# Kernel tuning notes

Measured on AMD Instinct MI355X. Metric: run time of the kernel, lower is better.

## Reference

```python
import jax, jax.numpy as jnp
import numpy as np

DIM = 768
HEADS = 12
FF = 3072
EPS = 1e-6


def setup_inputs() -> dict:
    key = jax.random.key(0)
    ks = jax.random.split(key, 12)
    B, S, D, F_ = 64, 197, DIM, FF
    s = 0.02
    inp = {
        "x": jax.random.normal(ks[0], (B, S, D), jnp.float32),
        "Wq": jax.random.normal(ks[1], (D, D), jnp.float32) * s,
        "bq": jnp.zeros((D,), jnp.float32),
        "Wk": jax.random.normal(ks[2], (D, D), jnp.float32) * s,
        "bk": jnp.zeros((D,), jnp.float32),
        "Wv": jax.random.normal(ks[3], (D, D), jnp.float32) * s,
        "bv": jnp.zeros((D,), jnp.float32),
        "Wo": jax.random.normal(ks[4], (D, D), jnp.float32) * s,
        "bo": jnp.zeros((D,), jnp.float32),
        "ln1_w": jnp.ones((D,), jnp.float32),
        "ln1_b": jnp.zeros((D,), jnp.float32),
        "W1": jax.random.normal(ks[5], (D, F_), jnp.float32) * s,
        "b1": jnp.zeros((F_,), jnp.float32),
        "W2": jax.random.normal(ks[6], (F_, D), jnp.float32) * s,
        "b2": jnp.zeros((D,), jnp.float32),
        "ln2_w": jnp.ones((D,), jnp.float32),
        "ln2_b": jnp.zeros((D,), jnp.float32),
        "mask": jnp.ones((B, S), jnp.int32),
    }
    return inp


def _layernorm(x, w, b):
    m = jnp.mean(x, axis=-1, keepdims=True)
    v = jnp.mean(jnp.square(x - m), axis=-1, keepdims=True)  # unbiased=False
    return (x - m) / jnp.sqrt(v + EPS) * w + b


def _block(x, mask_f, Wq, bq, Wk, bk, Wv, bv, Wo, bo, ln1_w, ln1_b, W1, b1, W2, b2, ln2_w, ln2_b):
    B, S, D = x.shape
    H = HEADS
    Dh = D // H
    # --- attention (pre-norm) ---
    h = _layernorm(x, ln1_w, ln1_b)
    q = (h @ Wq + bq).reshape(B, S, H, Dh).transpose(0, 2, 1, 3)
    k = (h @ Wk + bk).reshape(B, S, H, Dh).transpose(0, 2, 1, 3)
    v = (h @ Wv + bv).reshape(B, S, H, Dh).transpose(0, 2, 1, 3)
    scores = jnp.einsum("bhqd,bhkd->bhqk", q, k) / jnp.sqrt(jnp.float32(Dh))
    scores = scores - 10000.0 * (1.0 - mask_f[:, None, None, :])
    probs = jax.nn.softmax(scores, axis=-1)
    attn = jnp.einsum("bhqk,bhkd->bhqd", probs, v).transpose(0, 2, 1, 3).reshape(B, S, D)
    x = x + (attn @ Wo + bo)  # dropout = identity (eval)
    # --- FFN (pre-norm), exact erf GELU (F.gelu default) ---
    h = _layernorm(x, ln2_w, ln2_b)
    h = jax.nn.gelu(h @ W1 + b1, approximate=False)
    x = x + (h @ W2 + b2)
    return x


def reference(x, Wq, bq, Wk, bk, Wv, bv, Wo, bo, ln1_w, ln1_b, W1, b1, W2, b2, ln2_w, ln2_b, mask):
    mask_f = mask.astype(jnp.float32)
    return _block(x, mask_f, Wq, bq, Wk, bk, Wv, bv, Wo, bo, ln1_w, ln1_b, W1, b1, W2, b2, ln2_w, ln2_b)
```

## Files before the change

### kernel.cpp

```cpp
#include <hip/hip_runtime.h>
#include <stdint.h>

#define B_   64
#define S_   197
#define D_   768
#define H_   12
#define F_   3072
#define BS_  (B_ * S_)

typedef __attribute__((ext_vector_type(8))) short short8;
typedef __attribute__((ext_vector_type(4))) float f32x4;

__device__ __forceinline__ float bf2f(unsigned short h) {
    union { unsigned int u; float f; } v; v.u = ((unsigned int)h) << 16; return v.f;
}
__device__ __forceinline__ unsigned short f2bf(float f) {
    union { float f; unsigned int u; } v; v.f = f;
    unsigned int r = v.u + 0x7FFFu + ((v.u >> 16) & 1u);
    return (unsigned short)(r >> 16);
}

__device__ __forceinline__ void g2l16(const void* g, void* l) {
    __builtin_amdgcn_global_load_lds(
        (const __attribute__((address_space(1))) unsigned int*)g,
        (__attribute__((address_space(3))) unsigned int*)l, 16, 0, 0);
}

__global__ __launch_bounds__(256)
void transpose_w(const float* __restrict__ W, unsigned short* __restrict__ Wt, int K, int N) {
    __shared__ float t[32][33];
    int n0 = blockIdx.x * 32, k0 = blockIdx.y * 32;
    int tx = threadIdx.x, ty = threadIdx.y;
#pragma unroll
    for (int i = ty; i < 32; i += 8) t[i][tx] = W[(size_t)(k0 + i) * N + n0 + tx];
    __syncthreads();
#pragma unroll
    for (int i = ty; i < 32; i += 8) Wt[(size_t)(n0 + i) * K + k0 + tx] = f2bf(t[tx][i]);
}

__global__ void biascat_kernel(const float* bq, const float* bk, const float* bv, float* o) {
    int i = blockIdx.x * 256 + threadIdx.x;
    if (i < 2304) o[i] = i < 768 ? bq[i] : (i < 1536 ? bk[i - 768] : bv[i - 1536]);
}

__global__ __launch_bounds__(256)
void ln_kernel(const float* __restrict__ x, const float* __restrict__ w,
               const float* __restrict__ b, unsigned short* __restrict__ out) {
    int row = blockIdx.x; size_t base = (size_t)row * 768;
    int tid = threadIdx.x;
    float v0 = x[base + tid], v1 = x[base + tid + 256], v2 = x[base + tid + 512];
    float s1 = v0 + v1 + v2;
    float s2 = v0 * v0 + v1 * v1 + v2 * v2;
#pragma unroll
    for (int off = 32; off > 0; off >>= 1) { s1 += __shfl_xor(s1, off); s2 += __shfl_xor(s2, off); }
    __shared__ float sa[4], sb[4];
    int w4 = tid >> 6;
    if ((tid & 63) == 0) { sa[w4] = s1; sb[w4] = s2; }
    __syncthreads();
    s1 = sa[0] + sa[1] + sa[2] + sa[3];
    s2 = sb[0] + sb[1] + sb[2] + sb[3];
    float mean = s1 * (1.f / 768.f);
    float var  = s2 * (1.f / 768.f) - mean * mean;
    float rstd = rsqrtf(var + 1e-6f);
    out[base + tid]       = f2bf((v0 - mean) * rstd * w[tid]       + b[tid]);
    out[base + tid + 256] = f2bf((v1 - mean) * rstd * w[tid + 256] + b[tid + 256]);
    out[base + tid + 512] = f2bf((v2 - mean) * rstd * w[tid + 512] + b[tid + 512]);
}

template<int MODE>
__global__ __launch_bounds__(256)
void gemm_bf16(const unsigned short* __restrict__ A, const unsigned short* __restrict__ Bt,
               const float* __restrict__ bias, const float* __restrict__ resid,
               void* __restrict__ out, int M, int N, int K) {
    __shared__ unsigned short As[128 * 32];
    __shared__ unsigned short Bs[128 * 32];
    const int tid = threadIdx.x;
    const int l = tid & 63, w = tid >> 6;
    const int lr = l & 15, lg = l >> 4;
    const int wr = w >> 1, wc = w & 1;
    const int bm0 = blockIdx.y * 128, bn0 = blockIdx.x * 128;

    f32x4 acc[4][4];
#pragma unroll
    for (int i = 0; i < 4; ++i)
#pragma unroll
        for (int j = 0; j < 4; ++j) acc[i][j] = (f32x4){0.f, 0.f, 0.f, 0.f};

    for (int k0 = 0; k0 < K; k0 += 32) {
        __syncthreads();
#pragma unroll
        for (int p = 0; p < 2; ++p) {
            int r0 = p * 64 + w * 16;
            int ra = bm0 + r0 + (l >> 2); ra = ra < M ? ra : M - 1;
            g2l16(A + (size_t)ra * K + k0 + (l & 3) * 8, &As[r0 * 32]);
            int rb = bn0 + r0 + (l >> 2);
            g2l16(Bt + (size_t)rb * K + k0 + (l & 3) * 8, &Bs[r0 * 32]);
        }
        __syncthreads();
        short8 af[4], bfr[4];
#pragma unroll
        for (int i = 0; i < 4; ++i) af[i]  = *(const short8*)&As[(wr * 64 + i * 16 + lr) * 32 + lg * 8];
#pragma unroll
        for (int j = 0; j < 4; ++j) bfr[j] = *(const short8*)&Bs[(wc * 64 + j * 16 + lr) * 32 + lg * 8];
#pragma unroll
        for (int i = 0; i < 4; ++i)
#pragma unroll
            for (int j = 0; j < 4; ++j)
                acc[i][j] = __builtin_amdgcn_mfma_f32_16x16x32_bf16(af[i], bfr[j], acc[i][j], 0, 0, 0);
    }
#pragma unroll
    for (int i = 0; i < 4; ++i)
#pragma unroll
        for (int j = 0; j < 4; ++j)
#pragma unroll
            for (int r = 0; r < 4; ++r) {
                int gm = bm0 + wr * 64 + i * 16 + lg * 4 + r;
                int gn = bn0 + wc * 64 + j * 16 + lr;
                if (gm < M) {
                    float c = acc[i][j][r] + bias[gn];
                    if (MODE == 0) {
                        if (gn < 768) c *= 0.125f;
                        ((unsigned short*)out)[(size_t)gm * N + gn] = f2bf(c);
                    } else if (MODE == 1) {
                        ((float*)out)[(size_t)gm * N + gn] = c + resid[(size_t)gm * N + gn];
                    } else {
                        float g = 0.5f * c * (1.f + erff(c * 0.70710678118f));
                        ((unsigned short*)out)[(size_t)gm * N + gn] = f2bf(g);
                    }
                }
            }
}

__global__ __launch_bounds__(256)
void attn_mfma(const unsigned short* __restrict__ qkv, const int* __restrict__ mask,
               unsigned short* __restrict__ ctx) {
    __shared__ unsigned short Ks[208 * 64];
    __shared__ unsigned short Vt[64 * 256];
    __shared__ unsigned short Psl[4][16 * 40];
    __shared__ float maskadj[224];
    const int bh = blockIdx.x, b = bh / 12, h = bh - b * 12;
    const int tid = threadIdx.x, l = tid & 63, w = tid >> 6;
    const int lr = l & 15, lg = l >> 4;
    const unsigned short* Qg = qkv + (size_t)b * 197 * 2304 + h * 64;
    const unsigned short* Kg = Qg + 768;
    const unsigned short* Vg = Qg + 1536;

    if (tid < 224)
        maskadj[tid] = tid < 197 ? -10000.f * (1.f - (float)mask[b * 197 + tid]) : -1e30f;

    for (int c = w; c < 26; c += 4) {
        int row = c * 8 + (l >> 3);
        int rc = row < 197 ? row : 196;
        int blk = (l & 7) ^ (row & 7);
        g2l16(Kg + (size_t)rc * 2304 + blk * 8, &Ks[c * 8 * 64]);
    }
    {
        int jj = tid >> 3, db = tid & 7;
#pragma unroll
        for (int it = 0; it < 7; ++it) {
            int j = it * 32 + jj;
            short8 v = (short8){0, 0, 0, 0, 0, 0, 0, 0};
            if (j < 197) v = *(const short8*)(Vg + (size_t)j * 2304 + db * 8);
#pragma unroll
            for (int e = 0; e < 8; ++e) {
                int d = db * 8 + e;
                Vt[d * 256 + (((j >> 3) ^ (d & 7)) * 8) + (j & 7)] = (unsigned short)v[e];
            }
        }
    }
    __syncthreads();

    for (int t = w; t < 13; t += 4) {
        const int q0 = t * 16;
        int qr = q0 + lr; qr = qr < 197 ? qr : 196;
        const short8 qf0 = *(const short8*)(Qg + (size_t)qr * 2304 + lg * 8);
        const short8 qf1 = *(const short8*)(Qg + (size_t)qr * 2304 + 32 + lg * 8);

        f32x4 sc[13];
#pragma unroll
        for (int kt = 0; kt < 13; ++kt) {
            const int krow = kt * 16 + lr;
            const short8 kf0 = *(const short8*)&Ks[krow * 64 + ((lg ^ (lr & 7)) * 8)];
            const short8 kf1 = *(const short8*)&Ks[krow * 64 + (((4 + lg) ^ (lr & 7)) * 8)];
            f32x4 a = (f32x4){0.f, 0.f, 0.f, 0.f};
            a = __builtin_amdgcn_mfma_f32_16x16x32_bf16(qf0, kf0, a, 0, 0, 0);
            a = __builtin_amdgcn_mfma_f32_16x16x32_bf16(qf1, kf1, a, 0, 0, 0);
            sc[kt] = a;
        }
        float mx[4] = {-1e30f, -1e30f, -1e30f, -1e30f};
#pragma unroll
        for (int kt = 0; kt < 13; ++kt) {
            float ma = maskadj[kt * 16 + lr];
#pragma unroll
            for (int r = 0; r < 4; ++r) {
                sc[kt][r] += ma;
                mx[r] = fmaxf(mx[r], sc[kt][r]);
            }
        }
#pragma unroll
        for (int r = 0; r < 4; ++r) {
            mx[r] = fmaxf(mx[r], __shfl_xor(mx[r], 1));
            mx[r] = fmaxf(mx[r], __shfl_xor(mx[r], 2));
            mx[r] = fmaxf(mx[r], __shfl_xor(mx[r], 4));
            mx[r] = fmaxf(mx[r], __shfl_xor(mx[r], 8));
        }
        float sm[4] = {0.f, 0.f, 0.f, 0.f};
#pragma unroll
        for (int kt = 0; kt < 13; ++kt)
#pragma unroll
            for (int r = 0; r < 4; ++r) {
                float p = __expf(sc[kt][r] - mx[r]);
                sc[kt][r] = p;
                sm[r] += p;
            }
#pragma unroll
        for (int r = 0; r < 4; ++r) {
            sm[r] += __shfl_xor(sm[r], 1);
            sm[r] += __shfl_xor(sm[r], 2);
            sm[r] += __shfl_xor(sm[r], 4);
            sm[r] += __shfl_xor(sm[r], 8);
            sm[r] = 1.f / sm[r];
        }
        f32x4 ao[4];
#pragma unroll
        for (int dt = 0; dt < 4; ++dt) ao[dt] = (f32x4){0.f, 0.f, 0.f, 0.f};
        unsigned short* Pw = &Psl[w][0];
#pragma unroll
        for (int ks = 0; ks < 7; ++ks) {
#pragma unroll
            for (int tl = 0; tl < 2; ++tl) {
                const int kt = ks * 2 + tl;
#pragma unroll
                for (int r = 0; r < 4; ++r) {
                    unsigned short pv = 0;
                    if (kt < 13) pv = f2bf(sc[kt][r] * sm[r]);
                    Pw[(lg * 4 + r) * 40 + tl * 16 + lr] = pv;
                }
            }
            const short8 pf = *(const short8*)&Pw[lr * 40 + lg * 8];
#pragma unroll
            for (int dt = 0; dt < 4; ++dt) {
                const int drow = dt * 16 + lr;
                const short8 vf = *(const short8*)&Vt[drow * 256 + (((4 * ks + lg) ^ (lr & 7)) * 8)];
                ao[dt] = __builtin_amdgcn_mfma_f32_16x16x32_bf16(vf, pf, ao[dt], 0, 0, 0);
            }
        }
        const int q = q0 + lr;
        if (q < 197) {
            unsigned short* crow = ctx + ((size_t)b * 197 + q) * 768 + h * 64;
#pragma unroll
            for (int dt = 0; dt < 4; ++dt) {
                union { unsigned short u[4]; uint2 v; } pk;
#pragma unroll
                for (int r = 0; r < 4; ++r) pk.u[r] = f2bf(ao[dt][r]);
                *(uint2*)(crow + dt * 16 + lg * 4) = pk.v;
            }
        }
    }
}

extern "C" void kernel_launch(void* const* d_in, const int* in_sizes, int n_in,
                              void* d_out, int out_size, void* d_ws, size_t ws_size,
                              hipStream_t stream) {
    const float* x    = (const float*)d_in[0];
    const float* Wq   = (const float*)d_in[1];
    const float* bq   = (const float*)d_in[2];
    const float* Wk   = (const float*)d_in[3];
    const float* bk   = (const float*)d_in[4];
    const float* Wv   = (const float*)d_in[5];
    const float* bv   = (const float*)d_in[6];
    const float* Wo   = (const float*)d_in[7];
    const float* bo   = (const float*)d_in[8];
    const float* ln1w = (const float*)d_in[9];
    const float* ln1b = (const float*)d_in[10];
    const float* W1   = (const float*)d_in[11];
    const float* b1   = (const float*)d_in[12];
    const float* W2   = (const float*)d_in[13];
    const float* b2   = (const float*)d_in[14];
    const float* ln2w = (const float*)d_in[15];
    const float* ln2b = (const float*)d_in[16];
    const int*   mask = (const int*)d_in[17];

    size_t off = 0;
    auto nxt = [&](size_t bytes) -> void* {
        void* r = (char*)d_ws + off; off += (bytes + 255) & ~(size_t)255; return r;
    };
    unsigned short* hbuf  = (unsigned short*)nxt((size_t)BS_ * 768 * 2);
    unsigned short* qkvg  = (unsigned short*)nxt((size_t)BS_ * 3072 * 2);
    unsigned short* wqkvT = (unsigned short*)nxt((size_t)2304 * 768 * 2);
    unsigned short* woT   = (unsigned short*)nxt((size_t)768 * 768 * 2);
    unsigned short* w1T   = (unsigned short*)nxt((size_t)3072 * 768 * 2);
    unsigned short* w2T   = (unsigned short*)nxt((size_t)768 * 3072 * 2);
    float*          bcat  = (float*)nxt(2304 * 4);
    unsigned short* ctx   = (unsigned short*)nxt((size_t)BS_ * 768 * 2);
    (void)ws_size; (void)in_sizes; (void)n_in; (void)out_size;

    dim3 t32(32, 8, 1);
    transpose_w<<<dim3(24, 24), t32, 0, stream>>>(Wq, wqkvT,                 768, 768);
    transpose_w<<<dim3(24, 24), t32, 0, stream>>>(Wk, wqkvT + 768 * 768,     768, 768);
    transpose_w<<<dim3(24, 24), t32, 0, stream>>>(Wv, wqkvT + 2 * 768 * 768, 768, 768);
    transpose_w<<<dim3(24, 24), t32, 0, stream>>>(Wo, woT,                   768, 768);
    transpose_w<<<dim3(96, 24), t32, 0, stream>>>(W1, w1T,                   768, 3072);
    transpose_w<<<dim3(24, 96), t32, 0, stream>>>(W2, w2T,                   3072, 768);
    biascat_kernel<<<9, 256, 0, stream>>>(bq, bk, bv, bcat);

    ln_kernel<<<BS_, 256, 0, stream>>>(x, ln1w, ln1b, hbuf);
    gemm_bf16<0><<<dim3(18, 99), 256, 0, stream>>>(hbuf, wqkvT, bcat, nullptr, qkvg, BS_, 2304, 768);
    attn_mfma<<<768, 256, 0, stream>>>(qkvg, mask, ctx);
    gemm_bf16<1><<<dim3(6, 99), 256, 0, stream>>>(ctx, woT, bo, x, d_out, BS_, 768, 768);
    ln_kernel<<<BS_, 256, 0, stream>>>((const float*)d_out, ln2w, ln2b, hbuf);
    gemm_bf16<2><<<dim3(24, 99), 256, 0, stream>>>(hbuf, w1T, b1, nullptr, qkvg, BS_, 3072, 768);
    gemm_bf16<1><<<dim3(6, 99), 256, 0, stream>>>(qkvg, w2T, b2, (const float*)d_out, d_out, BS_, 768, 3072);
}
```

Measured before the change: 506.6 us.

## Double-buffer GEMM LDS tiles, swizzle LDS, remap XCDs, fuse weight prep kernels

The GEMM now uses two LDS buffers so the global-to-LDS load of the next K tile can overlap the MFMA work on the current one. It also XOR-swizzles the LDS column blocks to cut bank conflicts and remaps workgroup IDs so neighbouring M tiles land on the same XCD, which should improve L2 reuse of B tiles. Separately, the seven weight-transpose and bias-concat launches are merged into one kernel to reduce launch overhead. The cost is doubled LDS per block, which may lower occupancy, and a single sync per iteration that relies on the async load finishing in order.

```diff
diff --git a/kernel.cpp b/kernel.cpp
--- a/kernel.cpp
+++ b/kernel.cpp
@@ -27,20 +27,38 @@
 }
 
 __global__ __launch_bounds__(256)
-void transpose_w(const float* __restrict__ W, unsigned short* __restrict__ Wt, int K, int N) {
+void transpose_all(const float* __restrict__ Wq, const float* __restrict__ Wk,
+                   const float* __restrict__ Wv, const float* __restrict__ Wo,
+                   const float* __restrict__ W1, const float* __restrict__ W2,
+                   const float* __restrict__ bq, const float* __restrict__ bk,
+                   const float* __restrict__ bv,
+                   unsigned short* __restrict__ wqkvT, unsigned short* __restrict__ woT,
+                   unsigned short* __restrict__ w1T, unsigned short* __restrict__ w2T,
+                   float* __restrict__ bcat) {
+    int blk = blockIdx.x;
+    int tx = threadIdx.x, ty = threadIdx.y;
+    if (blk == 6912) {
+        for (int i = ty * 32 + tx; i < 2304; i += 256)
+            bcat[i] = i < 768 ? bq[i] : (i < 1536 ? bk[i - 768] : bv[i - 1536]);
+        return;
+    }
+    const float* W; unsigned short* Wt; int K, N, rel, nx;
+    if (blk < 2304) {
+        int m = blk / 576; rel = blk - m * 576; K = 768; N = 768; nx = 24;
+        W  = m == 0 ? Wq : m == 1 ? Wk : m == 2 ? Wv : Wo;
+        Wt = m < 3 ? wqkvT + (size_t)m * 768 * 768 : woT;
+    } else if (blk < 4608) {
+        rel = blk - 2304; K = 768; N = 3072; nx = 96; W = W1; Wt = w1T;
+    } else {
+        rel = blk - 4608; K = 3072; N = 768; nx = 24; W = W2; Wt = w2T;
+    }
+    int n0 = (rel % nx) * 32, k0 = (rel / nx) * 32;
     __shared__ float t[32][33];
-    int n0 = blockIdx.x * 32, k0 = blockIdx.y * 32;
-    int tx = threadIdx.x, ty = threadIdx.y;
 #pragma unroll
     for (int i = ty; i < 32; i += 8) t[i][tx] = W[(size_t)(k0 + i) * N + n0 + tx];
     __syncthreads();
 #pragma unroll
     for (int i = ty; i < 32; i += 8) Wt[(size_t)(n0 + i) * K + k0 + tx] = f2bf(t[tx][i]);
-}
-
-__global__ void biascat_kernel(const float* bq, const float* bk, const float* bv, float* o) {
-    int i = blockIdx.x * 256 + threadIdx.x;
-    if (i < 2304) o[i] = i < 768 ? bq[i] : (i < 1536 ? bk[i - 768] : bv[i - 1536]);
 }
 
 __global__ __launch_bounds__(256)
@@ -72,41 +90,60 @@
 void gemm_bf16(const unsigned short* __restrict__ A, const unsigned short* __restrict__ Bt,
                const float* __restrict__ bias, const float* __restrict__ resid,
                void* __restrict__ out, int M, int N, int K) {
-    __shared__ unsigned short As[128 * 32];
-    __shared__ unsigned short Bs[128 * 32];
+    __shared__ unsigned short As[2][128 * 32];
+    __shared__ unsigned short Bs[2][128 * 32];
     const int tid = threadIdx.x;
     const int l = tid & 63, w = tid >> 6;
     const int lr = l & 15, lg = l >> 4;
     const int wr = w >> 1, wc = w & 1;
-    const int bm0 = blockIdx.y * 128, bn0 = blockIdx.x * 128;
-
-    f32x4 acc[4][4];
-#pragma unroll
-    for (int i = 0; i < 4; ++i)
-#pragma unroll
-        for (int j = 0; j < 4; ++j) acc[i][j] = (f32x4){0.f, 0.f, 0.f, 0.f};
-
-    for (int k0 = 0; k0 < K; k0 += 32) {
-        __syncthreads();
+
+    const int nMt = gridDim.y;
+    const int nwg = gridDim.x * gridDim.y;
+    const int orig = blockIdx.x + gridDim.x * blockIdx.y;
+    const int q8 = nwg >> 3, r8 = nwg & 7;
+    const int xcd = orig & 7, idx = orig >> 3;
+    const int wgid = (xcd < r8 ? xcd * (q8 + 1) : r8 * (q8 + 1) + (xcd - r8) * q8) + idx;
+    const int bm0 = (wgid % nMt) * 128;
+    const int bn0 = (wgid / nMt) * 128;
+
+    const int srow = l >> 2;
+    const int sblk = (l & 3) ^ ((l >> 3) & 3);
+    auto stage = [&](int buf, int k0) {
 #pragma unroll
         for (int p = 0; p < 2; ++p) {
             int r0 = p * 64 + w * 16;
-            int ra = bm0 + r0 + (l >> 2); ra = ra < M ? ra : M - 1;
-            g2l16(A + (size_t)ra * K + k0 + (l & 3) * 8, &As[r0 * 32]);
-            int rb = bn0 + r0 + (l >> 2);
-            g2l16(Bt + (size_t)rb * K + k0 + (l & 3) * 8, &Bs[r0 * 32]);
-        }
-        __syncthreads();
+            int ra = bm0 + r0 + srow; ra = ra < M ? ra : M - 1;
+            g2l16(A + (size_t)ra * K + k0 + sblk * 8, &As[buf][r0 * 32]);
+            int rb = bn0 + r0 + srow;
+            g2l16(Bt + (size_t)rb * K + k0 + sblk * 8, &Bs[buf][r0 * 32]);
+        }
+    };
+
+    f32x4 acc[4][4];
+#pragma unroll
+    for (int i = 0; i < 4; ++i)
+#pragma unroll
+        for (int j = 0; j < 4; ++j) acc[i][j] = (f32x4){0.f, 0.f, 0.f, 0.f};
+
+    stage(0, 0);
+    __syncthreads();
+    int cur = 0;
+    const int NK = K >> 5;
+    const int rblk = lg ^ ((lr >> 1) & 3);
+    for (int kt = 0; kt < NK; ++kt) {
+        if (kt + 1 < NK) stage(cur ^ 1, (kt + 1) << 5);
         short8 af[4], bfr[4];
 #pragma unroll
-        for (int i = 0; i < 4; ++i) af[i]  = *(const short8*)&As[(wr * 64 + i * 16 + lr) * 32 + lg * 8];
-#pragma unroll
-        for (int j = 0; j < 4; ++j) bfr[j] = *(const short8*)&Bs[(wc * 64 + j * 16 + lr) * 32 + lg * 8];
+        for (int i = 0; i < 4; ++i) af[i]  = *(const short8*)&As[cur][(wr * 64 + i * 16 + lr) * 32 + rblk * 8];
+#pragma unroll
+        for (int j = 0; j < 4; ++j) bfr[j] = *(const short8*)&Bs[cur][(wc * 64 + j * 16 + lr) * 32 + rblk * 8];
 #pragma unroll
         for (int i = 0; i < 4; ++i)
 #pragma unroll
             for (int j = 0; j < 4; ++j)
                 acc[i][j] = __builtin_amdgcn_mfma_f32_16x16x32_bf16(af[i], bfr[j], acc[i][j], 0, 0, 0);
+        __syncthreads();
+        cur ^= 1;
     }
 #pragma unroll
     for (int i = 0; i < 4; ++i)
@@ -295,15 +332,8 @@
     unsigned short* ctx   = (unsigned short*)nxt((size_t)BS_ * 768 * 2);
     (void)ws_size; (void)in_sizes; (void)n_in; (void)out_size;
 
-    dim3 t32(32, 8, 1);
-    transpose_w<<<dim3(24, 24), t32, 0, stream>>>(Wq, wqkvT,                 768, 768);
-    transpose_w<<<dim3(24, 24), t32, 0, stream>>>(Wk, wqkvT + 768 * 768,     768, 768);
-    transpose_w<<<dim3(24, 24), t32, 0, stream>>>(Wv, wqkvT + 2 * 768 * 768, 768, 768);
-    transpose_w<<<dim3(24, 24), t32, 0, stream>>>(Wo, woT,                   768, 768);
-    transpose_w<<<dim3(96, 24), t32, 0, stream>>>(W1, w1T,                   768, 3072);
-    transpose_w<<<dim3(24, 96), t32, 0, stream>>>(W2, w2T,                   3072, 768);
-    biascat_kernel<<<9, 256, 0, stream>>>(bq, bk, bv, bcat);
-
+    transpose_all<<<6913, dim3(32, 8), 0, stream>>>(Wq, Wk, Wv, Wo, W1, W2, bq, bk, bv,
+                                                    wqkvT, woT, w1T, w2T, bcat);
     ln_kernel<<<BS_, 256, 0, stream>>>(x, ln1w, ln1b, hbuf);
     gemm_bf16<0><<<dim3(18, 99), 256, 0, stream>>>(hbuf, wqkvT, bcat, nullptr, qkvg, BS_, 2304, 768);
     attn_mfma<<<768, 256, 0, stream>>>(qkvg, mask, ctx);
```

Result: faster. 482.8 us (-4.7%).
